# Kernel optimization log

Hardware: AMD Instinct MI355X
Metric: run time of the kernel (lower is better)

The kernel has to match this reference:

```python
import jax, jax.numpy as jnp
import numpy as np
import math

N, M, K = 384, 32, 32  # x1 is (1, N, M, K)
DIM = 1                # init arg; scaled_qk = qk.div(1/sqrt(dim)) == qk * sqrt(dim)
DROP_P = 0.1


def setup_inputs() -> dict:
    key = jax.random.key(0)
    k1, k2 = jax.random.split(key)
    x1 = jax.random.normal(k1, (1, N, M, K), dtype=jnp.float32)
    # Deterministic dropout keep-mask, pre-scaled by 1/(1-p) (inverted dropout).
    u = jax.random.uniform(k2, (N, N, M, M), dtype=jnp.float32)
    dropout_mask = (u >= DROP_P).astype(jnp.float32) / (1.0 - DROP_P)
    return {"x1": x1, "dropout_mask": dropout_mask}


def reference(x1, dropout_mask):
    scale = math.sqrt(DIM)  # div by (1/sqrt(dim))
    query = x1                                   # (1, N, M, K)
    key_t = jnp.transpose(x1, (1, 0, 2, 3))      # (N, 1, M, K)
    # qk: broadcast batched matmul -> (N, N, M, M)
    qk = jnp.matmul(query, jnp.swapaxes(key_t, -2, -1))
    attn = jax.nn.softmax(qk * scale, axis=-1)   # (N, N, M, M)
    dropped = attn * dropout_mask                # dropout (training=True)
    # value = x1 (1, N, M, K) broadcasts -> output (N, N, M, K)
    out = jnp.matmul(dropped, x1)
    return out
```

## Files before the change

kernel.cpp:

```cpp
#include <hip/hip_runtime.h>
#include <hip/hip_bf16.h>

#define NN 384
#define MM 32
#define KK 32

typedef __attribute__((ext_vector_type(8))) __bf16 bf16x8;
typedef __attribute__((ext_vector_type(4))) float f32x4;

__device__ __forceinline__ void split8(const float* v, bf16x8& hi, bf16x8& lo) {
#pragma unroll
    for (int t = 0; t < 8; ++t) {
        float f = v[t];
        __bf16 h = (__bf16)f;
        hi[t] = h;
        lo[t] = (__bf16)(f - (float)h);
    }
}

__global__ __launch_bounds__(256) void attn_pair_kernel(
    const float* __restrict__ x1,
    const float* __restrict__ mask,
    float* __restrict__ out)
{
    __shared__ __align__(16) float  sST[4][32 * 36];
    __shared__ __align__(16) __bf16 sPhi[4][32 * 40];
    __shared__ __align__(16) __bf16 sPlo[4][32 * 40];

    const int tid  = threadIdx.x;
    const int w    = tid >> 6;
    const int l    = tid & 63;
    const int m16  = l & 15;
    const int quad = l >> 4;

    const unsigned p = blockIdx.x * 4u + (unsigned)w;
    const unsigned i = p / NN;
    const unsigned j = p - i * NN;

    const float* Q  = x1 + (size_t)j * (MM * KK);
    const float* Kt = x1 + (size_t)i * (MM * KK);

    bf16x8 aQh[2], aQl[2], bKh[2], bKl[2];
#pragma unroll
    for (int h = 0; h < 2; ++h) {
        const int row = h * 16 + m16;
        float qbuf[8], kbuf[8];
        *(float4*)&qbuf[0] = *(const float4*)(Q  + row * KK + quad * 8);
        *(float4*)&qbuf[4] = *(const float4*)(Q  + row * KK + quad * 8 + 4);
        *(float4*)&kbuf[0] = *(const float4*)(Kt + row * KK + quad * 8);
        *(float4*)&kbuf[4] = *(const float4*)(Kt + row * KK + quad * 8 + 4);
        split8(qbuf, aQh[h], aQl[h]);
        split8(kbuf, bKh[h], bKl[h]);
    }

    f32x4 S[2][2];
#pragma unroll
    for (int ma = 0; ma < 2; ++ma)
#pragma unroll
        for (int nb = 0; nb < 2; ++nb) {
            f32x4 c = {0.f, 0.f, 0.f, 0.f};
            c = __builtin_amdgcn_mfma_f32_16x16x32_bf16(aQl[ma], bKh[nb], c, 0, 0, 0);
            c = __builtin_amdgcn_mfma_f32_16x16x32_bf16(aQh[ma], bKl[nb], c, 0, 0, 0);
            c = __builtin_amdgcn_mfma_f32_16x16x32_bf16(aQh[ma], bKh[nb], c, 0, 0, 0);
            S[ma][nb] = c;
        }

#pragma unroll
    for (int ma = 0; ma < 2; ++ma)
#pragma unroll
        for (int nb = 0; nb < 2; ++nb) {
            const int b  = nb * 16 + m16;
            const int a0 = ma * 16 + quad * 4;
            *(f32x4*)&sST[w][b * 36 + a0] = S[ma][nb];
        }

    __syncthreads();

    const int a  = l >> 1;
    const int b0 = (l & 1) * 16;
    float s[16];
#pragma unroll
    for (int t = 0; t < 16; ++t) s[t] = sST[w][(b0 + t) * 36 + a];

    float mx = s[0];
#pragma unroll
    for (int t = 1; t < 16; ++t) mx = fmaxf(mx, s[t]);
    mx = fmaxf(mx, __shfl_xor(mx, 1, 64));

    float sum = 0.f;
#pragma unroll
    for (int t = 0; t < 16; ++t) { s[t] = __expf(s[t] - mx); sum += s[t]; }
    sum += __shfl_xor(sum, 1, 64);
    const float rinv = 1.0f / sum;

    const float* mrow = mask + (size_t)p * (MM * MM) + a * MM + b0;
    float mk[16];
    *(float4*)&mk[0]  = *(const float4*)(mrow + 0);
    *(float4*)&mk[4]  = *(const float4*)(mrow + 4);
    *(float4*)&mk[8]  = *(const float4*)(mrow + 8);
    *(float4*)&mk[12] = *(const float4*)(mrow + 12);

    float pv[16];
#pragma unroll
    for (int t = 0; t < 16; ++t) pv[t] = s[t] * rinv * mk[t];

    bf16x8 ph, plo;
    split8(&pv[0], ph, plo);
    *(bf16x8*)&sPhi[w][a * 40 + b0] = ph;
    *(bf16x8*)&sPlo[w][a * 40 + b0] = plo;
    split8(&pv[8], ph, plo);
    *(bf16x8*)&sPhi[w][a * 40 + b0 + 8] = ph;
    *(bf16x8*)&sPlo[w][a * 40 + b0 + 8] = plo;

    __syncthreads();

    bf16x8 aPh[2], aPl[2], bVh[2], bVl[2];
#pragma unroll
    for (int h = 0; h < 2; ++h) {
        aPh[h] = *(const bf16x8*)&sPhi[w][(h * 16 + m16) * 40 + quad * 8];
        aPl[h] = *(const bf16x8*)&sPlo[w][(h * 16 + m16) * 40 + quad * 8];
        const float* vp = Q + (quad * 8) * KK + (h * 16 + m16);
        float vbuf[8];
#pragma unroll
        for (int jj = 0; jj < 8; ++jj) vbuf[jj] = vp[jj * KK];
        split8(vbuf, bVh[h], bVl[h]);
    }

    f32x4 O[2][2];
#pragma unroll
    for (int ma = 0; ma < 2; ++ma)
#pragma unroll
        for (int nk = 0; nk < 2; ++nk) {
            f32x4 c = {0.f, 0.f, 0.f, 0.f};
            c = __builtin_amdgcn_mfma_f32_16x16x32_bf16(aPl[ma], bVh[nk], c, 0, 0, 0);
            c = __builtin_amdgcn_mfma_f32_16x16x32_bf16(aPh[ma], bVl[nk], c, 0, 0, 0);
            c = __builtin_amdgcn_mfma_f32_16x16x32_bf16(aPh[ma], bVh[nk], c, 0, 0, 0);
            O[ma][nk] = c;
        }

    float* obase = out + (size_t)p * (MM * KK);
#pragma unroll
    for (int ma = 0; ma < 2; ++ma)
#pragma unroll
        for (int nk = 0; nk < 2; ++nk) {
            const int col = nk * 16 + m16;
            const int r0  = ma * 16 + quad * 4;
#pragma unroll
            for (int rr = 0; rr < 4; ++rr)
                obase[(r0 + rr) * KK + col] = O[ma][nk][rr];
        }
}

extern "C" void kernel_launch(void* const* d_in, const int* in_sizes, int n_in,
                              void* d_out, int out_size, void* d_ws, size_t ws_size,
                              hipStream_t stream) {
    const float* x1   = (const float*)d_in[0];
    const float* mask = (const float*)d_in[1];
    float* out = (float*)d_out;
    const int pairs = NN * NN;
    dim3 grid(pairs / 4), block(256);
    attn_pair_kernel<<<grid, block, 0, stream>>>(x1, mask, out);
}
```

Baseline: 1.003 ms.

## Compute softmax in MFMA register layout and drop block barriers

```diff
diff --git a/kernel.cpp b/kernel.cpp
--- a/kernel.cpp
+++ b/kernel.cpp
@@ -6,6 +6,7 @@
 #define KK 32
 
 typedef __attribute__((ext_vector_type(8))) __bf16 bf16x8;
+typedef __attribute__((ext_vector_type(4))) __bf16 bf16x4;
 typedef __attribute__((ext_vector_type(4))) float f32x4;
 
 __device__ __forceinline__ void split8(const float* v, bf16x8& hi, bf16x8& lo) {
@@ -18,12 +19,21 @@
     }
 }
 
+__device__ __forceinline__ void split4(const float* v, bf16x4& hi, bf16x4& lo) {
+#pragma unroll
+    for (int t = 0; t < 4; ++t) {
+        float f = v[t];
+        __bf16 h = (__bf16)f;
+        hi[t] = h;
+        lo[t] = (__bf16)(f - (float)h);
+    }
+}
+
 __global__ __launch_bounds__(256) void attn_pair_kernel(
     const float* __restrict__ x1,
     const float* __restrict__ mask,
     float* __restrict__ out)
 {
-    __shared__ __align__(16) float  sST[4][32 * 36];
     __shared__ __align__(16) __bf16 sPhi[4][32 * 40];
     __shared__ __align__(16) __bf16 sPlo[4][32 * 40];
 
@@ -40,6 +50,14 @@
     const float* Q  = x1 + (size_t)j * (MM * KK);
     const float* Kt = x1 + (size_t)i * (MM * KK);
 
+    const float* mbase = mask + (size_t)p * (MM * MM);
+    f32x4 mk[2][2];
+#pragma unroll
+    for (int aa = 0; aa < 2; ++aa)
+#pragma unroll
+        for (int bb = 0; bb < 2; ++bb)
+            mk[aa][bb] = *(const f32x4*)(mbase + (aa * 16 + m16) * MM + bb * 16 + quad * 4);
+
     bf16x8 aQh[2], aQl[2], bKh[2], bKl[2];
 #pragma unroll
     for (int h = 0; h < 2; ++h) {
@@ -53,77 +71,75 @@
         split8(kbuf, bKh[h], bKl[h]);
     }
 
-    f32x4 S[2][2];
+    f32x4 ST[2][2];
 #pragma unroll
-    for (int ma = 0; ma < 2; ++ma)
+    for (int bb = 0; bb < 2; ++bb)
 #pragma unroll
-        for (int nb = 0; nb < 2; ++nb) {
+        for (int aa = 0; aa < 2; ++aa) {
             f32x4 c = {0.f, 0.f, 0.f, 0.f};
-            c = __builtin_amdgcn_mfma_f32_16x16x32_bf16(aQl[ma], bKh[nb], c, 0, 0, 0);
-            c = __builtin_amdgcn_mfma_f32_16x16x32_bf16(aQh[ma], bKl[nb], c, 0, 0, 0);
-            c = __builtin_amdgcn_mfma_f32_16x16x32_bf16(aQh[ma], bKh[nb], c, 0, 0, 0);
-            S[ma][nb] = c;
+            c = __builtin_amdgcn_mfma_f32_16x16x32_bf16(bKl[bb], aQh[aa], c, 0, 0, 0);
+            c = __builtin_amdgcn_mfma_f32_16x16x32_bf16(bKh[bb], aQl[aa], c, 0, 0, 0);
+            c = __builtin_amdgcn_mfma_f32_16x16x32_bf16(bKh[bb], aQh[aa], c, 0, 0, 0);
+            ST[bb][aa] = c;
         }
 
+    float pv[2][2][4];
 #pragma unroll
-    for (int ma = 0; ma < 2; ++ma)
+    for (int aa = 0; aa < 2; ++aa) {
+        float mx = ST[0][aa][0];
 #pragma unroll
-        for (int nb = 0; nb < 2; ++nb) {
-            const int b  = nb * 16 + m16;
-            const int a0 = ma * 16 + quad * 4;
-            *(f32x4*)&sST[w][b * 36 + a0] = S[ma][nb];
+        for (int bb = 0; bb < 2; ++bb)
+#pragma unroll
+            for (int r = 0; r < 4; ++r) mx = fmaxf(mx, ST[bb][aa][r]);
+        mx = fmaxf(mx, __shfl_xor(mx, 16, 64));
+        mx = fmaxf(mx, __shfl_xor(mx, 32, 64));
+
+        float sum = 0.f;
+#pragma unroll
+        for (int bb = 0; bb < 2; ++bb)
+#pragma unroll
+            for (int r = 0; r < 4; ++r) {
+                float e = __expf(ST[bb][aa][r] - mx);
+                pv[aa][bb][r] = e;
+                sum += e;
+            }
+        sum += __shfl_xor(sum, 16, 64);
+        sum += __shfl_xor(sum, 32, 64);
+        const float rinv = 1.0f / sum;
+#pragma unroll
+        for (int bb = 0; bb < 2; ++bb)
+#pragma unroll
+            for (int r = 0; r < 4; ++r)
+                pv[aa][bb][r] *= rinv * mk[aa][bb][r];
+    }
+
+#pragma unroll
+    for (int aa = 0; aa < 2; ++aa)
+#pragma unroll
+        for (int bb = 0; bb < 2; ++bb) {
+            bf16x4 h4, l4;
+            split4(pv[aa][bb], h4, l4);
+            const int off = (aa * 16 + m16) * 40 + bb * 16 + quad * 4;
+            *(bf16x4*)&sPhi[w][off] = h4;
+            *(bf16x4*)&sPlo[w][off] = l4;
         }
 
-    __syncthreads();
+    float vbuf[2][8];
+#pragma unroll
+    for (int h = 0; h < 2; ++h) {
+        const float* vp = Q + (quad * 8) * KK + (h * 16 + m16);
+#pragma unroll
+        for (int jj = 0; jj < 8; ++jj) vbuf[h][jj] = vp[jj * KK];
+    }
 
-    const int a  = l >> 1;
-    const int b0 = (l & 1) * 16;
-    float s[16];
-#pragma unroll
-    for (int t = 0; t < 16; ++t) s[t] = sST[w][(b0 + t) * 36 + a];
-
-    float mx = s[0];
-#pragma unroll
-    for (int t = 1; t < 16; ++t) mx = fmaxf(mx, s[t]);
-    mx = fmaxf(mx, __shfl_xor(mx, 1, 64));
-
-    float sum = 0.f;
-#pragma unroll
-    for (int t = 0; t < 16; ++t) { s[t] = __expf(s[t] - mx); sum += s[t]; }
-    sum += __shfl_xor(sum, 1, 64);
-    const float rinv = 1.0f / sum;
-
-    const float* mrow = mask + (size_t)p * (MM * MM) + a * MM + b0;
-    float mk[16];
-    *(float4*)&mk[0]  = *(const float4*)(mrow + 0);
-    *(float4*)&mk[4]  = *(const float4*)(mrow + 4);
-    *(float4*)&mk[8]  = *(const float4*)(mrow + 8);
-    *(float4*)&mk[12] = *(const float4*)(mrow + 12);
-
-    float pv[16];
-#pragma unroll
-    for (int t = 0; t < 16; ++t) pv[t] = s[t] * rinv * mk[t];
-
-    bf16x8 ph, plo;
-    split8(&pv[0], ph, plo);
-    *(bf16x8*)&sPhi[w][a * 40 + b0] = ph;
-    *(bf16x8*)&sPlo[w][a * 40 + b0] = plo;
-    split8(&pv[8], ph, plo);
-    *(bf16x8*)&sPhi[w][a * 40 + b0 + 8] = ph;
-    *(bf16x8*)&sPlo[w][a * 40 + b0 + 8] = plo;
-
-    __syncthreads();
+    asm volatile("s_waitcnt lgkmcnt(0)" ::: "memory");
 
     bf16x8 aPh[2], aPl[2], bVh[2], bVl[2];
 #pragma unroll
     for (int h = 0; h < 2; ++h) {
         aPh[h] = *(const bf16x8*)&sPhi[w][(h * 16 + m16) * 40 + quad * 8];
         aPl[h] = *(const bf16x8*)&sPlo[w][(h * 16 + m16) * 40 + quad * 8];
-        const float* vp = Q + (quad * 8) * KK + (h * 16 + m16);
-        float vbuf[8];
-#pragma unroll
-        for (int jj = 0; jj < 8; ++jj) vbuf[jj] = vp[jj * KK];
-        split8(vbuf, bVh[h], bVl[h]);
+        split8(vbuf[h], bVh[h], bVl[h]);
     }
 
     f32x4 O[2][2];
```

Measured after the change: 1.055 ms. 1.05x slower.
